# Performance work log

Hardware: AMD Instinct MI355X
Metric: run time of the kernel (lower is better)

Reference implementation:

```python
import jax, jax.numpy as jnp
import numpy as np

# Module hyperparameters (from init_kwargs)
IOU_T = 0.5
PROB_T = 0.75
COV = 10.0
TOPK = 500       # self.topk
PRE_K = 2048     # fixed-shape cap on post-threshold candidates entering NMS
B, C, H, W = 4, 4, 160, 160


def setup_inputs() -> dict:
    key = jax.random.key(0)
    k1, k2 = jax.random.split(key)
    mask = jax.random.normal(k1, (B, C, H, W), dtype=jnp.float32)
    # scale bias so boxes have ~10px extent (realistic detections)
    bias = jax.random.normal(k2, (B, 4, H, W), dtype=jnp.float32) * 8.0
    return {"mask": mask, "bias": bias}


def _pos_grid(h, w):
    # equivalent of np.dstack(np.mgrid[0:h, 0:w]) -> [h, w, 2] with (y, x)
    yy, xx = jnp.meshgrid(jnp.arange(h), jnp.arange(w), indexing="ij")
    return jnp.stack([yy, xx], axis=-1).astype(jnp.float32)


def _pairwise_iou(b):
    # b: [K, 4] as (y1, x1, y2, x2); torchvision-style IoU (areas unclamped, inter clamped)
    area = (b[:, 2] - b[:, 0]) * (b[:, 3] - b[:, 1])
    lt = jnp.maximum(b[:, None, :2], b[None, :, :2])
    rb = jnp.minimum(b[:, None, 2:], b[None, :, 2:])
    wh = jnp.clip(rb - lt, 0.0)
    inter = wh[..., 0] * wh[..., 1]
    return inter / (area[:, None] + area[None, :] - inter)


def _nms_keep(iou, valid, thresh):
    # boxes are pre-sorted by descending score; greedy suppression
    K = iou.shape[0]
    idx = jnp.arange(K)
    def body(i, keep):
        sup = (iou[i] > thresh) & (idx > i) & keep[i]
        return keep & ~sup
    return jax.lax.fori_loop(0, K, body, valid)


def _per_image(mask_i, bias_i, pos):
    # mask_i: [C, h, w], bias_i: [4, h, w], pos: [h, w, 2]
    p = jax.nn.softmax(mask_i, axis=0)
    prob = jax.lax.stop_gradient(p.max(axis=0))          # prob.detach()
    cls = p.argmax(axis=0)
    frontal = (cls != 0) & (prob > PROB_T)               # [h, w]
    # boxes = pos tiled to (y,x,y,x) + bias.permute(0,2,3,1)
    boxes = jnp.concatenate([pos, pos], axis=-1) + jnp.transpose(bias_i, (1, 2, 0))
    boxes = boxes.reshape(-1, 4)                          # [h*w, 4]
    score = jnp.where(frontal.reshape(-1), prob.reshape(-1), -1.0)
    # fixed-size candidate set, sorted by descending score (invalid -> -1)
    top_s, idx = jax.lax.top_k(score, PRE_K)
    cand = boxes[idx]
    valid = top_s > 0.0                                   # valid scores > PROB_T > 0
    keep = _nms_keep(_pairwise_iou(cand), valid, IOU_T)
    kept_s = jnp.where(keep, top_s, -1.0)
    fin_s, fi = jax.lax.top_k(kept_s, TOPK)               # min(topk, n) via padding
    fboxes = cand[fi]                                     # [TOPK, 4]
    fvalid = fin_s > 0.0
    fprob = jnp.where(fvalid, fin_s, 0.0)
    mu = (fboxes[:, :2] + fboxes[:, 2:]) * 0.5            # [TOPK, 2]
    sigma = fboxes[:, 2:] - fboxes[:, :2]
    sigma = jnp.where(fvalid[:, None], sigma, 1.0)        # safe divisor for padding
    # gaussian2d: z = (pos - mu) / (sigma / cov); heat = max_n exp(-|z|^2/2) * prob
    z = (pos[None] - mu[:, None, None, :]) / (sigma[:, None, None, :] / COV)  # [TOPK,h,w,2]
    g = jnp.exp(-0.5 * (z ** 2).sum(axis=-1)) * fprob[:, None, None]
    heat = g.max(axis=0)                                  # [h, w]; all-padded -> 0, matches n==0 case
    return heat, fboxes, fvalid


def reference(mask, bias):
    pos = _pos_grid(mask.shape[2], mask.shape[3])
    heat, fboxes, fvalid = jax.vmap(lambda m, b: _per_image(m, b, pos))(mask, bias)
    # original returns (heatmaps, mask, boxes); boxes padded to [B, TOPK, 4] with validity mask
    return heat, mask, fboxes, fvalid
```

## Files before the change

### kernel.cpp

```cpp
#include <hip/hip_runtime.h>
#include <math.h>

#define BATCH 4
#define NCH 4
#define H 160
#define W 160
#define NPIX (H * W)
#define PRE_K 2048
#define TOPK 500
#define PROB_T 0.75f
#define IOU_T 0.5f
#define COV 10.0f

#define SCORE_OFF 0u
#define KEY_OFF   409600u
#define F_OFF     1228800u
#define CSC_OFF   1261632u
#define CBOX_OFF  1294400u
#define SUP_OFF   1425472u
#define NV_OFF    3523648u
#define PAR_OFF   3523712u
#define FLAG_OFF  3563712u

#define OUT_HEAT_OFF 0
#define OUT_MASK_OFF 102400
#define OUT_BOX_OFF  512000
#define OUT_VAL_OFF  520000

typedef unsigned long long u64;
typedef unsigned int u32;

__device__ __forceinline__ int block_scan_excl(int v, int tid, int* tmp, int* total) {
    tmp[tid] = v;
    __syncthreads();
    for (int off = 1; off < 256; off <<= 1) {
        int y = (tid >= off) ? tmp[tid - off] : 0;
        __syncthreads();
        tmp[tid] += y;
        __syncthreads();
    }
    int incl = tmp[tid];
    *total = tmp[255];
    __syncthreads();
    return incl - v;
}

__global__ void k_score(const float* __restrict__ mask, float* __restrict__ score,
                        float* __restrict__ out_mask) {
    int b = blockIdx.y;
    int pix = blockIdx.x * 256 + threadIdx.x;
    const float* mp = mask + (size_t)b * NCH * NPIX + pix;
    float* op = out_mask + (size_t)b * NCH * NPIX + pix;
    float x0 = mp[0], x1 = mp[NPIX], x2 = mp[2 * NPIX], x3 = mp[3 * NPIX];
    op[0] = x0; op[NPIX] = x1; op[2 * NPIX] = x2; op[3 * NPIX] = x3;
    float m = x0; int c = 0;
    if (x1 > m) { m = x1; c = 1; }
    if (x2 > m) { m = x2; c = 2; }
    if (x3 > m) { m = x3; c = 3; }
    float sum = ((expf(x0 - m) + expf(x1 - m)) + expf(x2 - m)) + expf(x3 - m);
    float prob = 1.0f / sum;
    bool frontal = (c != 0) && (prob > PROB_T);
    score[(size_t)b * NPIX + pix] = frontal ? prob : -1.0f;
}

#define PPT (NPIX / 1024)
__global__ void __launch_bounds__(1024)
k_compact(const float* __restrict__ score, const float* __restrict__ bias,
          u64* __restrict__ keys, int* __restrict__ Fout,
          float* __restrict__ cand_score, float* __restrict__ cand_box) {
    int b = blockIdx.x;
    int tid = threadIdx.x;
    const float* sc = score + (size_t)b * NPIX;
    const float* bb = bias + (size_t)b * 4 * NPIX;
    int p0 = tid * PPT;
    float v[PPT];
    int cnt = 0;
    #pragma unroll
    for (int j = 0; j < PPT; ++j) {
        v[j] = sc[p0 + j];
        cnt += (v[j] > 0.0f) ? 1 : 0;
    }
    int lane = tid & 63, wv = tid >> 6;
    int incl = cnt;
    for (int off = 1; off < 64; off <<= 1) {
        int y = __shfl_up(incl, off);
        if (lane >= off) incl += y;
    }
    __shared__ int wtot[16];
    __shared__ int wpre[17];
    if (lane == 63) wtot[wv] = incl;
    __syncthreads();
    if (tid == 0) {
        int acc = 0;
        for (int k = 0; k < 16; ++k) { wpre[k] = acc; acc += wtot[k]; }
        wpre[16] = acc;
    }
    __syncthreads();
    int f_excl = wpre[wv] + (incl - cnt);
    int F = wpre[16];
    if (tid == 0) Fout[b] = F;
    int w = f_excl;
    #pragma unroll
    for (int j = 0; j < PPT; ++j) {
        if (v[j] > 0.0f) {
            u32 lo = 0x7FFFFFFFu - (u32)(p0 + j);
            keys[(size_t)b * NPIX + w] = ((u64)__float_as_uint(v[j]) << 32) | (u64)lo;
            ++w;
        }
    }
    if (F < PRE_K) {
        int slot = F + (p0 - f_excl);
        #pragma unroll
        for (int j = 0; j < PPT; ++j) {
            if (!(v[j] > 0.0f)) {
                if (slot < PRE_K) {
                    int pix = p0 + j;
                    cand_score[(size_t)b * PRE_K + slot] = -1.0f;
                    float y = (float)(pix / W), x = (float)(pix % W);
                    float4 box;
                    box.x = y + bb[0 * NPIX + pix];
                    box.y = x + bb[1 * NPIX + pix];
                    box.z = y + bb[2 * NPIX + pix];
                    box.w = x + bb[3 * NPIX + pix];
                    ((float4*)cand_box)[(size_t)b * PRE_K + slot] = box;
                }
                ++slot;
            }
        }
    }
}

#define RK_CH 4096
__global__ void k_rank(const u64* __restrict__ keys, const float* __restrict__ bias,
                       const int* __restrict__ Fout, float* __restrict__ cand_score,
                       float* __restrict__ cand_box) {
    int b = blockIdx.y;
    int F = Fout[b];
    if (blockIdx.x * 256 >= F) return;
    int i = blockIdx.x * 256 + threadIdx.x;
    const u64* kb = keys + (size_t)b * NPIX;
    u64 ki = (i < F) ? kb[i] : 0;
    int rank = 0;
    __shared__ u64 ks[RK_CH];
    for (int base = 0; base < F; base += RK_CH) {
        int lim = min(RK_CH, F - base);
        __syncthreads();
        for (int k = threadIdx.x; k < lim; k += 256) ks[k] = kb[base + k];
        __syncthreads();
        if (i < F) {
            int k = 0;
            for (; k + 8 <= lim; k += 8) {
                rank += (ks[k]     > ki) ? 1 : 0;
                rank += (ks[k + 1] > ki) ? 1 : 0;
                rank += (ks[k + 2] > ki) ? 1 : 0;
                rank += (ks[k + 3] > ki) ? 1 : 0;
                rank += (ks[k + 4] > ki) ? 1 : 0;
                rank += (ks[k + 5] > ki) ? 1 : 0;
                rank += (ks[k + 6] > ki) ? 1 : 0;
                rank += (ks[k + 7] > ki) ? 1 : 0;
            }
            for (; k < lim; ++k) rank += (ks[k] > ki) ? 1 : 0;
        }
    }
    if (i < F && rank < PRE_K) {
        float si = __uint_as_float((u32)(ki >> 32));
        int xi = 0x7FFFFFFF - (int)(u32)(ki & 0xFFFFFFFFu);
        cand_score[(size_t)b * PRE_K + rank] = si;
        const float* bb = bias + (size_t)b * 4 * NPIX;
        float y = (float)(xi / W), x = (float)(xi % W);
        float4 box;
        box.x = y + bb[0 * NPIX + xi];
        box.y = x + bb[1 * NPIX + xi];
        box.z = y + bb[2 * NPIX + xi];
        box.w = x + bb[3 * NPIX + xi];
        ((float4*)cand_box)[(size_t)b * PRE_K + rank] = box;
    }
}

__global__ void __launch_bounds__(512)
k_iou(const float* __restrict__ cand_box, const int* __restrict__ Fout,
      u32* __restrict__ sup, unsigned char* __restrict__ flag) {
    int b = blockIdx.y;
    int F = Fout[b];
    int V = F < PRE_K ? F : PRE_K;
    int r0 = blockIdx.x * 8;
    if (r0 >= V) return;
    __shared__ float ly1[PRE_K], lx1[PRE_K], ly2[PRE_K], lx2[PRE_K], lar[PRE_K];
    for (int k = threadIdx.x; k < PRE_K; k += 512) {
        float4 v = ((const float4*)cand_box)[(size_t)b * PRE_K + k];
        ly1[k] = v.x; lx1[k] = v.y; ly2[k] = v.z; lx2[k] = v.w;
        lar[k] = (v.z - v.x) * (v.w - v.y);
    }
    __syncthreads();
    int lr = threadIdx.x >> 6;
    int w = threadIdx.x & 63;
    int i = r0 + lr;
    float ay1 = ly1[i], ax1 = lx1[i], ay2 = ly2[i], ax2 = lx2[i], aa = lar[i];
    u32 bits = 0;
    int jbase = w * 32;
    #pragma unroll 4
    for (int jj = 0; jj < 32; ++jj) {
        int jo = (jj + w) & 31;
        int j = jbase + jo;
        if (j > i) {
            float lty = fmaxf(ay1, ly1[j]);
            float ltx = fmaxf(ax1, lx1[j]);
            float rby = fminf(ay2, ly2[j]);
            float rbx = fminf(ax2, lx2[j]);
            float wy = fmaxf(rby - lty, 0.0f);
            float wx = fmaxf(rbx - ltx, 0.0f);
            float inter = wy * wx;
            float iou = inter / ((aa + lar[j]) - inter);
            if (iou > IOU_T) bits |= (1u << jo);
        }
    }
    sup[((size_t)b * PRE_K + i) * 64 + w] = bits;
    bool any = __any(bits != 0u);
    if (w == 0) flag[(size_t)b * PRE_K + i] = any ? 1 : 0;
}

__global__ void __launch_bounds__(256)
k_nmsfin(const u32* __restrict__ sup, const unsigned char* __restrict__ flag,
         const int* __restrict__ Fout, const float* __restrict__ cand_score,
         const float* __restrict__ cand_box, float* __restrict__ out_boxes,
         float* __restrict__ out_valid, float* __restrict__ params,
         int* __restrict__ NV) {
    int b = blockIdx.x;
    int tid = threadIdx.x;
    int F = Fout[b];
    int V = F < PRE_K ? F : PRE_K;
    __shared__ int rid_s[PRE_K];
    __shared__ int M_s;
    __shared__ u32 kws[64];
    __shared__ int tmp[256];

    if (tid < 64) {
        int lane = tid;
        const u32* f32 = (const u32*)(flag + (size_t)b * PRE_K);
        u32 fw[8];
        #pragma unroll
        for (int k = 0; k < 8; ++k) fw[k] = f32[lane * 8 + k];
        int r0 = lane * 32;
        int cnt = 0;
        #pragma unroll
        for (int k = 0; k < 8; ++k)
            #pragma unroll
            for (int j = 0; j < 4; ++j) {
                int r = r0 + k * 4 + j;
                if (((fw[k] >> (8 * j)) & 0xFFu) != 0u && r < V) ++cnt;
            }
        int incl = cnt;
        for (int off = 1; off < 64; off <<= 1) {
            int y = __shfl_up(incl, off);
            if (lane >= off) incl += y;
        }
        if (lane == 63) M_s = incl;
        int pos = incl - cnt;
        #pragma unroll
        for (int k = 0; k < 8; ++k)
            #pragma unroll
            for (int j = 0; j < 4; ++j) {
                int r = r0 + k * 4 + j;
                if (((fw[k] >> (8 * j)) & 0xFFu) != 0u && r < V) rid_s[pos++] = r;
            }
    }
    __syncthreads();

    if (tid < 64) {
        int lane = tid;
        int M = M_s;
        int rem = V - lane * 32;
        u32 kw = (rem >= 32) ? 0xFFFFFFFFu : (rem <= 0 ? 0u : ((1u << rem) - 1u));
        const u32* supb = sup + (size_t)b * PRE_K * 64 + lane;
        int C = (M + 7) >> 3;
        int C4 = (C + 3) & ~3;
        int l7 = lane & 7;
        u32 rbuf[4][8];
        int ridv[4];

        #define LOAD_RID(slot, c) ridv[slot] = rid_s[min((c) * 8 + l7, PRE_K - 1)]
        #define ISSUE(slot) do { \
            _Pragma("unroll") \
            for (int k_ = 0; k_ < 8; ++k_) { \
                int i_ = __builtin_amdgcn_readlane(ridv[slot], k_) & (PRE_K - 1); \
                rbuf[slot][k_] = supb[(size_t)i_ * 64]; \
            } \
        } while (0)
        #define PROC(slot, c) do { \
            _Pragma("unroll") \
            for (int k_ = 0; k_ < 8; ++k_) { \
                int m_ = (c) * 8 + k_; \
                if (m_ < M) { \
                    int i_ = __builtin_amdgcn_readlane(ridv[slot], k_) & (PRE_K - 1); \
                    u32 kb_ = (u32)__builtin_amdgcn_readlane((int)kw, i_ >> 5); \
                    if ((kb_ >> (i_ & 31)) & 1u) kw &= ~rbuf[slot][k_]; \
                } \
            } \
        } while (0)

        LOAD_RID(0, 0); LOAD_RID(1, 1); LOAD_RID(2, 2); LOAD_RID(3, 3);
        ISSUE(0); ISSUE(1); ISSUE(2);
        for (int c = 0; c < C4; c += 4) {
            PROC(0, c);     ISSUE(3);            LOAD_RID(0, c + 4);
            PROC(1, c + 1); ISSUE(0);            LOAD_RID(1, c + 5);
            PROC(2, c + 2); ISSUE(1);            LOAD_RID(2, c + 6);
            PROC(3, c + 3); ISSUE(2);            LOAD_RID(3, c + 7);
        }
        #undef LOAD_RID
        #undef ISSUE
        #undef PROC
        kws[lane] = kw;
    }
    __syncthreads();

    int s0 = tid * 8;
    int bits8 = (int)((kws[s0 >> 5] >> (s0 & 31)) & 0xFFu);
    int cnt = __popc(bits8);
    int tot;
    int kpre = block_scan_excl(cnt, tid, tmp, &tot);
    int NK = tot;
    for (int k = 0; k < 8; ++k) {
        int s = s0 + k;
        int kept = (bits8 >> k) & 1;
        int pos = kept ? kpre : (NK + s - kpre);
        if (pos < TOPK) {
            float4 bx = ((const float4*)cand_box)[(size_t)b * PRE_K + s];
            ((float4*)out_boxes)[(size_t)b * TOPK + pos] = bx;
            out_valid[(size_t)b * TOPK + pos] = kept ? 1.0f : 0.0f;
            if (kept) {
                float scv = cand_score[(size_t)b * PRE_K + s];
                float* pp = params + ((size_t)b * TOPK + pos) * 5;
                pp[0] = (bx.x + bx.z) * 0.5f;
                pp[1] = (bx.y + bx.w) * 0.5f;
                pp[2] = (bx.z - bx.x) / COV;
                pp[3] = (bx.w - bx.y) / COV;
                pp[4] = scv;
            }
        }
        kpre += kept;
    }
    if (tid == 0) NV[b] = NK < TOPK ? NK : TOPK;
}

#define TILE 16
#define TPL (W / TILE)
__global__ void k_heat(const float* __restrict__ params, const int* __restrict__ NV,
                       float* __restrict__ heat) {
    int b = blockIdx.y;
    int ty0 = (blockIdx.x / TPL) * TILE;
    int tx0 = (blockIdx.x % TPL) * TILE;
    int tid = threadIdx.x;
    int nv = NV[b];
    __shared__ float lp[TOPK * 5];
    __shared__ int cntS;
    if (tid == 0) cntS = 0;
    __syncthreads();
    for (int t = tid; t < nv; t += 256) {
        const float* pp = params + ((size_t)b * TOPK + t) * 5;
        float muy = pp[0], mux = pp[1], dy = pp[2], dx = pp[3], p = pp[4];
        float cy = fmaxf(fmaxf((float)ty0 - muy, muy - (float)(ty0 + TILE - 1)), 0.0f);
        float cx = fmaxf(fmaxf((float)tx0 - mux, mux - (float)(tx0 + TILE - 1)), 0.0f);
        float zy = cy / fabsf(dy);
        float zx = cx / fabsf(dx);
        float z2 = zy * zy + zx * zx;
        if (!(z2 > 40.0f)) {
            int idx = atomicAdd(&cntS, 1);
            float* q = lp + idx * 5;
            q[0] = muy; q[1] = mux; q[2] = dy; q[3] = dx; q[4] = p;
        }
    }
    __syncthreads();
    int n = cntS;
    float py = (float)(ty0 + (tid >> 4));
    float px = (float)(tx0 + (tid & 15));
    float m = 0.0f;
    for (int t = 0; t < n; ++t) {
        float muy = lp[t * 5 + 0], mux = lp[t * 5 + 1];
        float dy = lp[t * 5 + 2], dx = lp[t * 5 + 3], p = lp[t * 5 + 4];
        float zy = (py - muy) / dy;
        float zx = (px - mux) / dx;
        float g = expf(-0.5f * (zy * zy + zx * zx)) * p;
        m = fmaxf(m, g);
    }
    heat[(size_t)b * NPIX + (ty0 + (tid >> 4)) * W + tx0 + (tid & 15)] = m;
}

extern "C" void kernel_launch(void* const* d_in, const int* in_sizes, int n_in,
                              void* d_out, int out_size, void* d_ws, size_t ws_size,
                              hipStream_t stream) {
    const float* mask = (const float*)d_in[0];
    const float* bias = (const float*)d_in[1];
    float* out = (float*)d_out;
    char* ws = (char*)d_ws;

    float* score      = (float*)(ws + SCORE_OFF);
    u64*   keys       = (u64*)(ws + KEY_OFF);
    int*   Fout       = (int*)(ws + F_OFF);
    float* cand_score = (float*)(ws + CSC_OFF);
    float* cand_box   = (float*)(ws + CBOX_OFF);
    u32*   sup        = (u32*)(ws + SUP_OFF);
    int*   NV         = (int*)(ws + NV_OFF);
    float* params     = (float*)(ws + PAR_OFF);
    unsigned char* flag = (unsigned char*)(ws + FLAG_OFF);

    dim3 g100(NPIX / 256, BATCH);
    k_score<<<g100, 256, 0, stream>>>(mask, score, out + OUT_MASK_OFF);
    k_compact<<<BATCH, 1024, 0, stream>>>(score, bias, keys, Fout, cand_score, cand_box);
    k_rank<<<g100, 256, 0, stream>>>(keys, bias, Fout, cand_score, cand_box);
    k_iou<<<dim3(PRE_K / 8, BATCH), 512, 0, stream>>>(cand_box, Fout, sup, flag);
    k_nmsfin<<<BATCH, 256, 0, stream>>>(sup, flag, Fout, cand_score, cand_box,
                                        out + OUT_BOX_OFF, out + OUT_VAL_OFF, params, NV);
    k_heat<<<dim3(TPL * (H / TILE), BATCH), 256, 0, stream>>>(params, NV, out + OUT_HEAT_OFF);
}
```

Measured before the change: 118.5 us.

## Parallelize stream compaction across tiles using per-block counts from score kernel

```diff
diff --git a/kernel.cpp b/kernel.cpp
--- a/kernel.cpp
+++ b/kernel.cpp
@@ -6,6 +6,7 @@
 #define H 160
 #define W 160
 #define NPIX (H * W)
+#define NTILE (NPIX / 256)
 #define PRE_K 2048
 #define TOPK 500
 #define PROB_T 0.75f
@@ -21,6 +22,7 @@
 #define NV_OFF    3523648u
 #define PAR_OFF   3523712u
 #define FLAG_OFF  3563712u
+#define BCNT_OFF  3571904u
 
 #define OUT_HEAT_OFF 0
 #define OUT_MASK_OFF 102400
@@ -46,7 +48,7 @@
 }
 
 __global__ void k_score(const float* __restrict__ mask, float* __restrict__ score,
-                        float* __restrict__ out_mask) {
+                        float* __restrict__ out_mask, int* __restrict__ blkcnt) {
     int b = blockIdx.y;
     int pix = blockIdx.x * 256 + threadIdx.x;
     const float* mp = mask + (size_t)b * NCH * NPIX + pix;
@@ -61,71 +63,70 @@
     float prob = 1.0f / sum;
     bool frontal = (c != 0) && (prob > PROB_T);
     score[(size_t)b * NPIX + pix] = frontal ? prob : -1.0f;
-}
-
-#define PPT (NPIX / 1024)
-__global__ void __launch_bounds__(1024)
+    __shared__ int wcnt[4];
+    u64 bm = __ballot(frontal);
+    if ((threadIdx.x & 63) == 0) wcnt[threadIdx.x >> 6] = __popcll(bm);
+    __syncthreads();
+    if (threadIdx.x == 0)
+        blkcnt[b * NTILE + blockIdx.x] = wcnt[0] + wcnt[1] + wcnt[2] + wcnt[3];
+}
+
+__global__ void __launch_bounds__(256)
 k_compact(const float* __restrict__ score, const float* __restrict__ bias,
-          u64* __restrict__ keys, int* __restrict__ Fout,
-          float* __restrict__ cand_score, float* __restrict__ cand_box) {
-    int b = blockIdx.x;
+          const int* __restrict__ blkcnt, u64* __restrict__ keys,
+          int* __restrict__ Fout, float* __restrict__ cand_score,
+          float* __restrict__ cand_box) {
+    int b = blockIdx.y;
+    int bx = blockIdx.x;
     int tid = threadIdx.x;
-    const float* sc = score + (size_t)b * NPIX;
-    const float* bb = bias + (size_t)b * 4 * NPIX;
-    int p0 = tid * PPT;
-    float v[PPT];
-    int cnt = 0;
-    #pragma unroll
-    for (int j = 0; j < PPT; ++j) {
-        v[j] = sc[p0 + j];
-        cnt += (v[j] > 0.0f) ? 1 : 0;
-    }
+    const int* bc = blkcnt + b * NTILE;
+    int f_base = 0, F = 0;
+    #pragma unroll 4
+    for (int k = 0; k < NTILE; ++k) {
+        int c = bc[k];
+        F += c;
+        if (k < bx) f_base += c;
+    }
+    int pix = bx * 256 + tid;
+    float s = score[(size_t)b * NPIX + pix];
+    bool fr = (s > 0.0f);
     int lane = tid & 63, wv = tid >> 6;
-    int incl = cnt;
+    int v = fr ? 1 : 0;
+    int incl = v;
     for (int off = 1; off < 64; off <<= 1) {
         int y = __shfl_up(incl, off);
         if (lane >= off) incl += y;
     }
-    __shared__ int wtot[16];
-    __shared__ int wpre[17];
+    __shared__ int wtot[4];
+    __shared__ int wpre[4];
     if (lane == 63) wtot[wv] = incl;
     __syncthreads();
     if (tid == 0) {
         int acc = 0;
-        for (int k = 0; k < 16; ++k) { wpre[k] = acc; acc += wtot[k]; }
-        wpre[16] = acc;
-    }
-    __syncthreads();
-    int f_excl = wpre[wv] + (incl - cnt);
-    int F = wpre[16];
-    if (tid == 0) Fout[b] = F;
-    int w = f_excl;
-    #pragma unroll
-    for (int j = 0; j < PPT; ++j) {
-        if (v[j] > 0.0f) {
-            u32 lo = 0x7FFFFFFFu - (u32)(p0 + j);
-            keys[(size_t)b * NPIX + w] = ((u64)__float_as_uint(v[j]) << 32) | (u64)lo;
-            ++w;
-        }
-    }
-    if (F < PRE_K) {
-        int slot = F + (p0 - f_excl);
-        #pragma unroll
-        for (int j = 0; j < PPT; ++j) {
-            if (!(v[j] > 0.0f)) {
-                if (slot < PRE_K) {
-                    int pix = p0 + j;
-                    cand_score[(size_t)b * PRE_K + slot] = -1.0f;
-                    float y = (float)(pix / W), x = (float)(pix % W);
-                    float4 box;
-                    box.x = y + bb[0 * NPIX + pix];
-                    box.y = x + bb[1 * NPIX + pix];
-                    box.z = y + bb[2 * NPIX + pix];
-                    box.w = x + bb[3 * NPIX + pix];
-                    ((float4*)cand_box)[(size_t)b * PRE_K + slot] = box;
-                }
-                ++slot;
-            }
+        for (int k = 0; k < 4; ++k) { wpre[k] = acc; acc += wtot[k]; }
+    }
+    __syncthreads();
+    int f_local = wpre[wv] + (incl - v);
+    if (fr) {
+        u32 lo = 0x7FFFFFFFu - (u32)pix;
+        keys[(size_t)b * NPIX + f_base + f_local] =
+            ((u64)__float_as_uint(s) << 32) | (u64)lo;
+    }
+    if (bx == 0 && tid == 0) Fout[b] = F;
+    if (!fr) {
+        int nf_base = bx * 256 - f_base;
+        int nf_local = tid - f_local;
+        int slot = F + nf_base + nf_local;
+        if (slot < PRE_K) {
+            const float* bb = bias + (size_t)b * 4 * NPIX;
+            cand_score[(size_t)b * PRE_K + slot] = -1.0f;
+            float y = (float)(pix / W), x = (float)(pix % W);
+            float4 box;
+            box.x = y + bb[0 * NPIX + pix];
+            box.y = x + bb[1 * NPIX + pix];
+            box.z = y + bb[2 * NPIX + pix];
+            box.w = x + bb[3 * NPIX + pix];
+            ((float4*)cand_box)[(size_t)b * PRE_K + slot] = box;
         }
     }
 }
@@ -402,10 +403,12 @@
     int*   NV         = (int*)(ws + NV_OFF);
     float* params     = (float*)(ws + PAR_OFF);
     unsigned char* flag = (unsigned char*)(ws + FLAG_OFF);
-
-    dim3 g100(NPIX / 256, BATCH);
-    k_score<<<g100, 256, 0, stream>>>(mask, score, out + OUT_MASK_OFF);
-    k_compact<<<BATCH, 1024, 0, stream>>>(score, bias, keys, Fout, cand_score, cand_box);
+    int*   blkcnt     = (int*)(ws + BCNT_OFF);
+
+    dim3 g100(NTILE, BATCH);
+    k_score<<<g100, 256, 0, stream>>>(mask, score, out + OUT_MASK_OFF, blkcnt);
+    k_compact<<<g100, 256, 0, stream>>>(score, bias, blkcnt, keys, Fout,
+                                        cand_score, cand_box);
     k_rank<<<g100, 256, 0, stream>>>(keys, bias, Fout, cand_score, cand_box);
     k_iou<<<dim3(PRE_K / 8, BATCH), 512, 0, stream>>>(cand_box, Fout, sup, flag);
     k_nmsfin<<<BATCH, 256, 0, stream>>>(sup, flag, Fout, cand_score, cand_box,
```

New measurement: 115.5 us. 1.03x faster.
